# Kernel optimization log

Measured on AMD Instinct MI355X. Metric: run time of the kernel, lower is better.

The kernel has to match this reference:

```python
import jax, jax.numpy as jnp
import numpy as np
import math

HEADS = 2
DH = 64
INNER = HEADS * DH  # 128
TOPK = 128
ALPHA = 10.0
N_FREQ = 8  # feature_dim // (2*input_dim) = 64 // 8
OMEGAS = jnp.logspace(1.0, math.log10(128.0), N_FREQ)           # sigma_q = 128
OMEGAS_L = [jnp.logspace(1.0, math.log10(s), N_FREQ) for s in (128.0, 32.0)]
LAYER_NUM = 2


def calc_gamma(grid, omegas):
    # grid: (Q, 4) -> (Q, 4*2*n_freq)
    arg = jnp.pi * grid[:, :, None] * omegas[None, None, :]      # (Q,4,n)
    g = jnp.concatenate([jnp.sin(arg), jnp.cos(arg)], axis=-1)   # (Q,4,2n)
    return g.reshape(grid.shape[0], -1)


def setup_inputs() -> dict:
    key = jax.random.key(0)
    ks = jax.random.split(key, 20)
    B, Q, L, HD, FD, OD = 2, 4096, 1024, 256, 64, 1

    def w(k, shape, fan_in):
        return jax.random.normal(k, shape, dtype=jnp.float32) * (1.0 / np.sqrt(fan_in))

    inp = {
        'x': jax.random.uniform(ks[0], (B, Q, 4), dtype=jnp.float32),
        'tokens': jax.random.normal(ks[1], (B, L, HD), dtype=jnp.float32),
        'query_W': w(ks[2], (FD, HD), FD),
        'query_b': jnp.zeros((HD,), jnp.float32),
        'q_W': w(ks[3], (HD, INNER), HD),
        'kv_W': w(ks[4], (HD, 2 * INNER), HD),
        'out_W': w(ks[5], (INNER, HD), INNER),
        'out_b': jnp.zeros((HD,), jnp.float32),
        'band_W': w(ks[6], (LAYER_NUM, FD, HD), FD),
        'band_b': jnp.zeros((LAYER_NUM, HD), jnp.float32),
        'mod_W': w(ks[7], (LAYER_NUM, HD, HD), HD),
        'mod_b': jnp.zeros((LAYER_NUM, HD), jnp.float32),
        'hv_W': w(ks[8], (LAYER_NUM - 1, HD, HD), HD),
        'hv_b': jnp.zeros((LAYER_NUM - 1, HD), jnp.float32),
        'outl_W': w(ks[9], (LAYER_NUM, HD, OD), HD),
        'outl_b': jnp.zeros((LAYER_NUM, OD), jnp.float32),
        'gD': 8, 'gH': 8, 'gW': 8, 'gT': 8,
    }
    return inp


def reference(x, tokens, query_W, query_b, q_W, kv_W, out_W, out_b,
              band_W, band_b, mod_W, mod_b, hv_W, hv_b, outl_W, outl_b,
              gD, gH, gW, gT):
    B, Q, _ = x.shape
    L = tokens.shape[1]
    grid = x[0]  # (Q, 4) — torch code uses x[0] for all batches

    # --- patch index + approximate relative distances -> sparse attn indices ---
    z_i = (grid[:, 0] * gD).astype(jnp.int32)
    y_i = (grid[:, 1] * gH).astype(jnp.int32)
    x_i = (grid[:, 2] * gW).astype(jnp.int32)
    t_i = (grid[:, 3] * gT).astype(jnp.int32)
    idx = ((t_i * gD + z_i) * gH + y_i) * gW + x_i               # (Q,)
    N = gD * gH * gW * gT
    t = idx / N                                                  # (Q,) float
    tok_pos = (jnp.arange(L, dtype=jnp.float32) + 0.5) / L       # (L,)
    bias = ALPHA * (t[:, None] - tok_pos[None, :]) ** 2          # (Q, L)
    # top-k SMALLEST distances (identical across batch, compute once)
    _, attn_idx = jax.lax.top_k(-bias, TOPK)                     # (Q, k)

    # --- query features ---
    gamma_q = calc_gamma(grid, OMEGAS)                           # (Q, 64)
    x_q = jax.nn.relu(gamma_q @ query_W + query_b)               # (Q, 256)
    x_q = jnp.broadcast_to(x_q[None], (B, Q, x_q.shape[-1]))

    # --- sparse shared-token cross attention ---
    scale = DH ** -0.5
    q = (x_q @ q_W).reshape(B, Q, HEADS, DH)                     # (B,Q,H,Dh)
    kv = tokens @ kv_W                                           # (B,L,2*inner)
    k_full, v_full = kv[..., :INNER], kv[..., INNER:]            # (B,L,inner)
    k_sp = k_full[:, attn_idx, :].reshape(B, Q, TOPK, HEADS, DH)  # (B,Q,k,H,Dh)
    v_sp = v_full[:, attn_idx, :].reshape(B, Q, TOPK, HEADS, DH)
    sim = jnp.einsum('bqhd,bqkhd->bhqk', q, k_sp) * scale        # (B,H,Q,k)
    attn = jax.nn.softmax(sim, axis=-1)
    o = jnp.einsum('bhqk,bqkhd->bqhd', attn, v_sp).reshape(B, Q, INNER)
    modulation = o @ out_W + out_b                               # (B,Q,256)

    # --- per-band modulation ---
    mods = []
    for l in range(LAYER_NUM):
        gamma_l = calc_gamma(grid, OMEGAS_L[l])                  # (Q, 64)
        h_l = jax.nn.relu(gamma_l @ band_W[l] + band_b[l])       # (Q, 256)
        m_l = jax.nn.relu(h_l[None] + modulation @ mod_W[l] + mod_b[l])
        mods.append(m_l)

    h_v = [mods[0]]
    for i in range(LAYER_NUM - 1):
        h_v.append(jax.nn.relu((mods[i + 1] + h_v[i]) @ hv_W[i] + hv_b[i]))

    out = sum(h_v[i] @ outl_W[i] + outl_b[i] for i in range(LAYER_NUM))
    return out  # (B, Q, output_dim)
```

## Files before the change

### kernel.cpp

```cpp
#include <hip/hip_runtime.h>
#include <math.h>

#define BN     2
#define QN     4096
#define LN     1024
#define TOPKN  128
#define PI_F   3.14159265358979323846f

#define K_OM0  0.3642064529893673
#define K_OM1  0.1661644014008115

#define NCMAX  320
#define PFP    328

typedef __attribute__((ext_vector_type(8))) short  s16x8;
typedef __attribute__((ext_vector_type(4))) short  s16x4;
typedef __attribute__((ext_vector_type(4))) float  f32x4;
typedef unsigned short u16;

__device__ __forceinline__ u16 f2bf(float f) {
    unsigned int u = __float_as_uint(f);
    u = (u + 0x7FFFu + ((u >> 16) & 1u)) >> 16;
    return (u16)u;
}

__device__ __forceinline__ size_t wtile(int n, int k, int K) {
    return (size_t)((n >> 4) * (K >> 5) + (k >> 5)) * 512 + (n & 15) * 32 + (k & 31);
}
__device__ __forceinline__ size_t kidx(int b, int l, int d) {
    return (((size_t)(b * 64 + (l >> 4)) * 16 + (d >> 3)) * 16 + (l & 15)) * 8 + (d & 7);
}
__device__ __forceinline__ size_t vidx(int b, int n, int k) {
    return (((size_t)(b * 8 + (n >> 4)) * 128 + (k >> 3)) * 16 + (n & 15)) * 8 + (k & 7);
}

struct KvS { u16 tok[32 * 264]; u16 stage[256 * 40]; float vtile[128][40]; };
struct QS  { float shx[128]; u16 gam[32 * 72]; u16 xq[32 * 264]; u16 stage[256 * 40]; };
struct TrS { float tile[32][33]; };
struct SoS { int hist[1024]; int cur[1024]; };
union PrepS { KvS kv; QS q; TrS tr; SoS so; };

__global__ __launch_bounds__(1024) void prep_kernel(
    const float* __restrict__ tokens, const float* __restrict__ kv_W,
    const float* __restrict__ x, const float* __restrict__ query_W,
    const float* __restrict__ query_b, const float* __restrict__ q_W,
    const float* __restrict__ outW, const float* __restrict__ bandW,
    const float* __restrict__ modW, const float* __restrict__ hvW,
    const int* __restrict__ gDp, const int* __restrict__ gHp,
    const int* __restrict__ gWp, const int* __restrict__ gTp,
    float* __restrict__ qall, u16* __restrict__ kbf, u16* __restrict__ vtbf,
    u16* __restrict__ outT, u16* __restrict__ bandT,
    u16* __restrict__ modT, u16* __restrict__ hvT,
    int* __restrict__ perm, int* __restrict__ ssort)
{
    __shared__ __align__(16) PrepS sm;
    const int bid = blockIdx.x;
    const int t   = threadIdx.x;
    const int wid = t >> 6, lane = t & 63;
    const int quad = lane >> 4, l16 = lane & 15;

    if (bid < 64) {
        int l0 = bid * 32;
        int b = l0 >> 10, lloc = l0 & 1023;
        #pragma unroll
        for (int i = 0; i < 8; i++) {
            int idx = i * 1024 + t; int row = idx >> 8, col = idx & 255;
            sm.kv.tok[row * 264 + col] = f2bf(tokens[(size_t)(l0 + row) * 256 + col]);
        }
        int m0 = (wid & 1) * 16;
        int c0 = (wid >> 1) * 32;
        f32x4 acc[2];
        acc[0] = (f32x4){0.f, 0.f, 0.f, 0.f};
        acc[1] = (f32x4){0.f, 0.f, 0.f, 0.f};
        for (int kc = 0; kc < 8; kc++) {
            __syncthreads();
            #pragma unroll
            for (int i = 0; i < 8; i++) {
                int idx = i * 1024 + t; int k = idx >> 8, n = idx & 255;
                sm.kv.stage[n * 40 + k] = f2bf(kv_W[(size_t)(kc * 32 + k) * 256 + n]);
            }
            __syncthreads();
            s16x8 a = *(const s16x8*)&sm.kv.tok[(m0 + l16) * 264 + kc * 32 + quad * 8];
            #pragma unroll
            for (int sub = 0; sub < 2; sub++) {
                s16x8 bfr = *(const s16x8*)&sm.kv.stage[(c0 + sub * 16 + l16) * 40 + quad * 8];
                acc[sub] = __builtin_amdgcn_mfma_f32_16x16x32_bf16(a, bfr, acc[sub], 0, 0, 0);
            }
        }
        #pragma unroll
        for (int sub = 0; sub < 2; sub++) {
            int col = c0 + sub * 16 + l16;
            if (col < 128) {
                #pragma unroll
                for (int r = 0; r < 4; r++) {
                    int lg = l0 + m0 + quad * 4 + r;
                    kbf[kidx(lg >> 10, lg & 1023, col)] = f2bf(acc[sub][r]);
                }
            } else {
                #pragma unroll
                for (int r = 0; r < 4; r++)
                    sm.kv.vtile[col - 128][m0 + quad * 4 + r] = acc[sub][r];
            }
        }
        __syncthreads();
        {
            int col = t >> 3, rg = (t & 7) * 4;
            float4 v4 = *(const float4*)&sm.kv.vtile[col][rg];
            s16x4 pk;
            pk[0] = (short)f2bf(v4.x); pk[1] = (short)f2bf(v4.y);
            pk[2] = (short)f2bf(v4.z); pk[3] = (short)f2bf(v4.w);
            *(s16x4*)&vtbf[vidx(b, col, lloc + rg)] = pk;
        }
    } else if (bid < 192) {
        int p0 = (bid - 64) * 32;
        if (t < 128) sm.q.shx[t] = x[p0 * 4 + t];
        __syncthreads();
        #pragma unroll
        for (int j = 0; j < 2; j++) {
            int e = t * 2 + j;
            int g = e >> 6, f = e & 63;
            int c = f >> 4, jj = f & 15, oi = jj & 7;
            float om = (float)(10.0 * exp((double)oi * K_OM0));
            float arg = PI_F * sm.q.shx[g * 4 + c] * om;
            sm.q.gam[g * 72 + f] = f2bf((jj < 8) ? sinf(arg) : cosf(arg));
        }
        int m0 = (wid & 1) * 16;
        {
            int c0 = (wid >> 1) * 32;
            f32x4 acc[2];
            acc[0] = (f32x4){0.f, 0.f, 0.f, 0.f};
            acc[1] = (f32x4){0.f, 0.f, 0.f, 0.f};
            for (int kc = 0; kc < 2; kc++) {
                __syncthreads();
                #pragma unroll
                for (int i = 0; i < 8; i++) {
                    int idx = i * 1024 + t; int k = idx >> 8, n = idx & 255;
                    sm.q.stage[n * 40 + k] = f2bf(query_W[(size_t)(kc * 32 + k) * 256 + n]);
                }
                __syncthreads();
                s16x8 a = *(const s16x8*)&sm.q.gam[(m0 + l16) * 72 + kc * 32 + quad * 8];
                #pragma unroll
                for (int sub = 0; sub < 2; sub++) {
                    s16x8 bfr = *(const s16x8*)&sm.q.stage[(c0 + sub * 16 + l16) * 40 + quad * 8];
                    acc[sub] = __builtin_amdgcn_mfma_f32_16x16x32_bf16(a, bfr, acc[sub], 0, 0, 0);
                }
            }
            #pragma unroll
            for (int sub = 0; sub < 2; sub++) {
                int col = c0 + sub * 16 + l16;
                float bias = query_b[col];
                #pragma unroll
                for (int r = 0; r < 4; r++)
                    sm.q.xq[(m0 + quad * 4 + r) * 264 + col] = f2bf(fmaxf(acc[sub][r] + bias, 0.f));
            }
        }
        {
            int n0q = (wid >> 1) * 16;
            f32x4 acc2 = (f32x4){0.f, 0.f, 0.f, 0.f};
            for (int kc = 0; kc < 8; kc++) {
                __syncthreads();
                #pragma unroll
                for (int i = 0; i < 4; i++) {
                    int idx = i * 1024 + t; int k = idx >> 7, n = idx & 127;
                    sm.q.stage[n * 40 + k] = f2bf(q_W[(size_t)(kc * 32 + k) * 128 + n]);
                }
                __syncthreads();
                s16x8 a = *(const s16x8*)&sm.q.xq[(m0 + l16) * 264 + kc * 32 + quad * 8];
                s16x8 bfr = *(const s16x8*)&sm.q.stage[(n0q + l16) * 40 + quad * 8];
                acc2 = __builtin_amdgcn_mfma_f32_16x16x32_bf16(a, bfr, acc2, 0, 0, 0);
            }
            #pragma unroll
            for (int r = 0; r < 4; r++)
                qall[(size_t)(p0 + m0 + quad * 4 + r) * 128 + n0q + l16] = acc2[r];
        }
    } else if (bid < 448) {
        int bid2 = bid - 192;
        const float* src; u16* dst; int K, N, lt;
        if      (bid2 < 32)  { src = outW;  dst = outT;  K = 128; N = 256; lt = bid2; }
        else if (bid2 < 64)  { src = bandW; dst = bandT; K = 128; N = 256; lt = bid2 - 32; }
        else if (bid2 < 192) { src = modW;  dst = modT;  K = 512; N = 256; lt = bid2 - 64; }
        else                 { src = hvW;   dst = hvT;   K = 256; N = 256; lt = bid2 - 192; }
        int tk = K >> 5;
        int ktile = lt % tk, nt = lt / tk;
        int k0 = ktile * 32, n0 = nt * 32;
        int tx = t & 31, ty = (t >> 5) & 31;
        sm.tr.tile[ty][tx] = src[(size_t)(k0 + ty) * N + n0 + tx];
        __syncthreads();
        dst[wtile(n0 + ty, k0 + tx, K)] = f2bf(sm.tr.tile[tx][ty]);
    } else {
        int gD = gDp[0], gH = gHp[0], gW = gWp[0], gT = gTp[0];
        int Ng = gD * gH * gW * gT;
        sm.so.hist[t] = 0;
        __syncthreads();
        int sarr[4];
        #pragma unroll
        for (int i = 0; i < 4; i++) {
            int q = i * 1024 + t;
            float4 xv = *(const float4*)&x[q * 4];
            int zi = (int)(xv.x * (float)gD);
            int yi = (int)(xv.y * (float)gH);
            int xi = (int)(xv.z * (float)gW);
            int ti = (int)(xv.w * (float)gT);
            int idx = ((ti * gD + zi) * gH + yi) * gW + xi;
            float tt = (float)idx / (float)Ng;
            int s = (int)ceilf(tt * (float)LN - ((float)(TOPKN / 2) + 0.5f));
            s = min(max(s, 0), LN - TOPKN);
            sarr[i] = s;
            atomicAdd(&sm.so.hist[s], 1);
        }
        __syncthreads();
        int cnt = sm.so.hist[t];
        sm.so.cur[t] = cnt;
        __syncthreads();
        for (int off = 1; off < 1024; off <<= 1) {
            int u = (t >= off) ? sm.so.cur[t - off] : 0;
            __syncthreads();
            sm.so.cur[t] += u;
            __syncthreads();
        }
        int excl = sm.so.cur[t] - cnt;
        __syncthreads();
        sm.so.hist[t] = excl;
        __syncthreads();
        #pragma unroll
        for (int i = 0; i < 4; i++) {
            int q = i * 1024 + t;
            int pos = atomicAdd(&sm.so.hist[sarr[i]], 1);
            perm[pos] = q;
            ssort[pos] = sarr[i];
        }
    }
}

__global__ __launch_bounds__(1024, 8) void fused_kernel(
    const float* __restrict__ x,
    const u16* __restrict__ kbf, const u16* __restrict__ vtbf,
    const float* __restrict__ qall,
    const int* __restrict__ perm, const int* __restrict__ ssort,
    const u16* __restrict__ outT, const float* __restrict__ out_b,
    const u16* __restrict__ bandT, const float* __restrict__ band_b,
    const u16* __restrict__ modT, const float* __restrict__ mod_b,
    const u16* __restrict__ hvT, const float* __restrict__ hv_b,
    const float* __restrict__ outl_W, const float* __restrict__ outl_b,
    float* __restrict__ out)
{
    const int bid = blockIdx.x;
    const int b   = bid >> 8;
    const int sp0 = (bid & 255) * 16;
    const int t   = threadIdx.x;
    const int wid = t >> 6, lane = t & 63;
    const int quad = lane >> 4, l16 = lane & 15;

    __shared__ __align__(16) u16 q_bf[16 * 136];
    __shared__ __align__(16) u16 gam_lds[32 * 72];
    __shared__ __align__(16) u16 P_bf[32 * PFP];
    __shared__ __align__(16) unsigned char regionA[PFP * 16 * 4];
    __shared__ __align__(16) u16 o_lds[16 * 136];
    __shared__ float fin[256];
    __shared__ float sh_xc[64];
    __shared__ int sh_pq[16], sh_s[16];

    float* P_f32 = (float*)regionA;
    float* o_part = (float*)regionA;
    u16* modu_lds = (u16*)regionA;
    u16* s01_lds  = (u16*)(regionA + 16 * 264 * 2);

    if (t < 16) { sh_pq[t] = perm[sp0 + t]; sh_s[t] = ssort[sp0 + t]; }
    __syncthreads();

    {
        int m = t >> 6, d = (t & 63) * 2;
        float2 qv = *(const float2*)&qall[(size_t)sh_pq[m] * 128 + d];
        unsigned int pk = (unsigned int)f2bf(qv.x) | ((unsigned int)f2bf(qv.y) << 16);
        *(unsigned int*)&q_bf[m * 136 + d] = pk;
    }
    if (t < 64) sh_xc[t] = x[(size_t)sh_pq[t >> 2] * 4 + (t & 3)];
    __syncthreads();

    #pragma unroll
    for (int j = 0; j < 2; j++) {
        int e = t * 2 + j;
        int l = e >> 10, g = (e >> 6) & 15, f = e & 63;
        int c = f >> 4, jj = f & 15, oi = jj & 7;
        float om = (float)(10.0 * exp((double)oi * (l ? K_OM1 : K_OM0)));
        float arg = PI_F * sh_xc[g * 4 + c] * om;
        gam_lds[(l * 16 + g) * 72 + f] = f2bf((jj < 8) ? sinf(arg) : cosf(arg));
    }

    const int u0    = sh_s[0] & ~15;
    const int ncols = min((sh_s[15] + 128 - u0 + 31) & ~31, NCMAX);
    const int nsub  = ncols >> 4;
    const int nkc   = ncols >> 5;

    #pragma unroll
    for (int h = 0; h < 2; h++) {
        s16x8 aq0 = *(const s16x8*)&q_bf[l16 * 136 + h * 64 + quad * 8];
        s16x8 aq1 = *(const s16x8*)&q_bf[l16 * 136 + h * 64 + 32 + quad * 8];
        for (int sub = wid; sub < nsub; sub += 16) {
            f32x4 acc = (f32x4){0.f, 0.f, 0.f, 0.f};
            int lrow = u0 + sub * 16 + l16;
            s16x8 b0 = *(const s16x8*)&kbf[kidx(b, lrow, h * 64 + quad * 8)];
            s16x8 b1 = *(const s16x8*)&kbf[kidx(b, lrow, h * 64 + 32 + quad * 8)];
            acc = __builtin_amdgcn_mfma_f32_16x16x32_bf16(aq0, b0, acc, 0, 0, 0);
            acc = __builtin_amdgcn_mfma_f32_16x16x32_bf16(aq1, b1, acc, 0, 0, 0);
            #pragma unroll
            for (int r = 0; r < 4; r++)
                P_f32[(quad * 4 + r) * PFP + sub * 16 + l16] = acc[r];
        }
        __syncthreads();
        {
            int g = wid;
            int sg = sh_s[g];
            float vals[5]; int ok[5];
            float mx = -1e30f;
            #pragma unroll
            for (int i = 0; i < 5; i++) {
                int c = lane + 64 * i;
                float v = P_f32[g * PFP + c] * 0.125f;
                int key = u0 + c;
                int o2 = (c < ncols) && (key >= sg) && (key < sg + 128);
                vals[i] = v; ok[i] = o2;
                if (o2) mx = fmaxf(mx, v);
            }
            #pragma unroll
            for (int off = 1; off < 64; off <<= 1) mx = fmaxf(mx, __shfl_xor(mx, off));
            float sum = 0.f, e5[5];
            #pragma unroll
            for (int i = 0; i < 5; i++) {
                float e = ok[i] ? expf(vals[i] - mx) : 0.f;
                e5[i] = e; sum += e;
            }
            #pragma unroll
            for (int off = 1; off < 64; off <<= 1) sum += __shfl_xor(sum, off);
            float inv = 1.f / sum;
            #pragma unroll
            for (int i = 0; i < 5; i++) {
                int c = lane + 64 * i;
                if (c < ncols) P_bf[(h * 16 + g) * PFP + c] = f2bf(e5[i] * inv);
            }
        }
        __syncthreads();
    }

    {
        int n0 = (wid & 7) * 16;
        int hh = n0 >> 6;
        int khalf = wid >> 3;
        int nk2 = (nkc + 1) >> 1;
        int k0 = khalf ? nk2 : 0;
        int k1 = khalf ? nkc : nk2;
        f32x4 acc = (f32x4){0.f, 0.f, 0.f, 0.f};
        for (int kc = k0; kc < k1; kc++) {
            s16x8 a = *(const s16x8*)&P_bf[(hh * 16 + l16) * PFP + kc * 32 + quad * 8];
            int koff = u0 + kc * 32 + quad * 8;
            koff = min(koff, 1016);
            s16x8 bfr = *(const s16x8*)&vtbf[vidx(b, n0 + l16, koff)];
            acc = __builtin_amdgcn_mfma_f32_16x16x32_bf16(a, bfr, acc, 0, 0, 0);
        }
        #pragma unroll
        for (int r = 0; r < 4; r++)
            o_part[(khalf * 16 + quad * 4 + r) * 128 + n0 + l16] = acc[r];
    }
    __syncthreads();

    {
        int m = t >> 6, j2 = (t & 63) * 2;
        float v0 = o_part[m * 128 + j2]     + o_part[(16 + m) * 128 + j2];
        float v1 = o_part[m * 128 + j2 + 1] + o_part[(16 + m) * 128 + j2 + 1];
        unsigned int pk = (unsigned int)f2bf(v0) | ((unsigned int)f2bf(v1) << 16);
        *(unsigned int*)&o_lds[m * 136 + j2] = pk;
    }
    __syncthreads();

    const int n0 = wid * 16;
    float m0f[4];

    {
        f32x4 acc = (f32x4){0.f, 0.f, 0.f, 0.f};
        #pragma unroll
        for (int kc = 0; kc < 4; kc++) {
            s16x8 a = *(const s16x8*)&o_lds[l16 * 136 + kc * 32 + quad * 8];
            s16x8 bfr = *(const s16x8*)&outT[wtile(n0 + l16, kc * 32 + quad * 8, 128)];
            acc = __builtin_amdgcn_mfma_f32_16x16x32_bf16(a, bfr, acc, 0, 0, 0);
        }
        int col = n0 + l16;
        float bias = out_b[col];
        #pragma unroll
        for (int r = 0; r < 4; r++)
            modu_lds[(quad * 4 + r) * 264 + col] = f2bf(acc[r] + bias);
    }
    __syncthreads();

    #pragma unroll
    for (int l = 0; l < 2; l++) {
        f32x4 acc1 = (f32x4){0.f, 0.f, 0.f, 0.f};
        f32x4 acc2 = (f32x4){0.f, 0.f, 0.f, 0.f};
        #pragma unroll
        for (int kc = 0; kc < 2; kc++) {
            s16x8 a = *(const s16x8*)&gam_lds[(l * 16 + l16) * 72 + kc * 32 + quad * 8];
            s16x8 bfr = *(const s16x8*)&bandT[wtile(n0 + l16, l * 64 + kc * 32 + quad * 8, 128)];
            acc1 = __builtin_amdgcn_mfma_f32_16x16x32_bf16(a, bfr, acc1, 0, 0, 0);
        }
        #pragma unroll
        for (int kc = 0; kc < 8; kc++) {
            s16x8 a = *(const s16x8*)&modu_lds[l16 * 264 + kc * 32 + quad * 8];
            s16x8 bfr = *(const s16x8*)&modT[wtile(n0 + l16, l * 256 + kc * 32 + quad * 8, 512)];
            acc2 = __builtin_amdgcn_mfma_f32_16x16x32_bf16(a, bfr, acc2, 0, 0, 0);
        }
        int col = n0 + l16;
        float bb = band_b[l * 256 + col];
        float mb = mod_b[l * 256 + col];
        #pragma unroll
        for (int r = 0; r < 4; r++) {
            float hval = fmaxf(acc1[r] + bb, 0.f);
            float mval = fmaxf(hval + acc2[r] + mb, 0.f);
            if (l == 0) m0f[r] = mval;
            else s01_lds[(quad * 4 + r) * 264 + col] = f2bf(m0f[r] + mval);
        }
    }
    __syncthreads();

    {
        f32x4 acc = (f32x4){0.f, 0.f, 0.f, 0.f};
        #pragma unroll
        for (int kc = 0; kc < 8; kc++) {
            s16x8 a = *(const s16x8*)&s01_lds[l16 * 264 + kc * 32 + quad * 8];
            s16x8 bfr = *(const s16x8*)&hvT[wtile(n0 + l16, kc * 32 + quad * 8, 256)];
            acc = __builtin_amdgcn_mfma_f32_16x16x32_bf16(a, bfr, acc, 0, 0, 0);
        }
        int col = n0 + l16;
        float w0 = outl_W[col], w1 = outl_W[256 + col], hb = hv_b[col];
        #pragma unroll
        for (int r = 0; r < 4; r++) {
            float hvv = fmaxf(acc[r] + hb, 0.f);
            float pv = m0f[r] * w0 + hvv * w1;
            #pragma unroll
            for (int off = 1; off < 16; off <<= 1) pv += __shfl_xor(pv, off);
            if (l16 == 0) fin[wid * 16 + quad * 4 + r] = pv;
        }
    }
    __syncthreads();
    if (t < 16) {
        float s2 = outl_b[0] + outl_b[1];
        #pragma unroll
        for (int w = 0; w < 16; w++) s2 += fin[w * 16 + t];
        out[(size_t)b * QN + sh_pq[t]] = s2;
    }
}

extern "C" void kernel_launch(void* const* d_in, const int* in_sizes, int n_in,
                              void* d_out, int out_size, void* d_ws, size_t ws_size,
                              hipStream_t stream)
{
    const float* x       = (const float*)d_in[0];
    const float* tokens  = (const float*)d_in[1];
    const float* query_W = (const float*)d_in[2];
    const float* query_b = (const float*)d_in[3];
    const float* q_W     = (const float*)d_in[4];
    const float* kv_W    = (const float*)d_in[5];
    const float* out_W   = (const float*)d_in[6];
    const float* out_b   = (const float*)d_in[7];
    const float* band_W  = (const float*)d_in[8];
    const float* band_b  = (const float*)d_in[9];
    const float* mod_W   = (const float*)d_in[10];
    const float* mod_b   = (const float*)d_in[11];
    const float* hv_W    = (const float*)d_in[12];
    const float* hv_b    = (const float*)d_in[13];
    const float* outl_W  = (const float*)d_in[14];
    const float* outl_b  = (const float*)d_in[15];
    const int*   gD      = (const int*)d_in[16];
    const int*   gH      = (const int*)d_in[17];
    const int*   gW      = (const int*)d_in[18];
    const int*   gT      = (const int*)d_in[19];

    float* ws   = (float*)d_ws;
    float* qall = ws;
    u16* wb = (u16*)(ws + 524288);
    u16* kbf   = wb;
    u16* vtbf  = wb + 262144;
    u16* outT  = wb + 524288;
    u16* bandT = wb + 557056;
    u16* modT  = wb + 589824;
    u16* hvT   = wb + 720896;
    int* perm  = (int*)(wb + 786432);
    int* ssort = perm + 4096;
    float* out = (float*)d_out;

    prep_kernel<<<449, 1024, 0, stream>>>(tokens, kv_W, x, query_W, query_b, q_W,
                                          out_W, band_W, mod_W, hv_W,
                                          gD, gH, gW, gT,
                                          qall, kbf, vtbf, outT, bandT, modT, hvT,
                                          perm, ssort);
    fused_kernel<<<512, 1024, 0, stream>>>(x, kbf, vtbf, qall, perm, ssort,
        outT, out_b, bandT, band_b, modT, mod_b, hvT, hv_b,
        outl_W, outl_b, out);
}
```

Measured before the change: 130.0 us.

## Merge per-head score and softmax passes and drop split-K PV reduction

Both heads' QK score tiles are now computed in one loop into a single 32-row fp32 LDS buffer, followed by one softmax pass, which removes two barriers per block. Softmax probabilities are written as bf16 in place over the fp32 scores. The PV matmul drops its split-K across 16 waves: only 8 waves run the full K loop and write bf16 output directly, which removes the partial-sum buffer, the reduction step and one barrier. The trade-off is that half the waves sit idle during PV and each active wave runs a longer serial K loop.

```diff
diff --git a/kernel.cpp b/kernel.cpp
--- a/kernel.cpp
+++ b/kernel.cpp
@@ -253,17 +253,14 @@
 
     __shared__ __align__(16) u16 q_bf[16 * 136];
     __shared__ __align__(16) u16 gam_lds[32 * 72];
-    __shared__ __align__(16) u16 P_bf[32 * PFP];
-    __shared__ __align__(16) unsigned char regionA[PFP * 16 * 4];
+    __shared__ __align__(16) float scores32[32 * PFP];
     __shared__ __align__(16) u16 o_lds[16 * 136];
     __shared__ float fin[256];
     __shared__ float sh_xc[64];
     __shared__ int sh_pq[16], sh_s[16];
 
-    float* P_f32 = (float*)regionA;
-    float* o_part = (float*)regionA;
-    u16* modu_lds = (u16*)regionA;
-    u16* s01_lds  = (u16*)(regionA + 16 * 264 * 2);
+    u16* modu_lds = (u16*)scores32;
+    u16* s01_lds  = ((u16*)scores32) + 16 * 264;
 
     if (t < 16) { sh_pq[t] = perm[sp0 + t]; sh_s[t] = ssort[sp0 + t]; }
     __syncthreads();
@@ -292,31 +289,39 @@
     const int nsub  = ncols >> 4;
     const int nkc   = ncols >> 5;
 
-    #pragma unroll
-    for (int h = 0; h < 2; h++) {
-        s16x8 aq0 = *(const s16x8*)&q_bf[l16 * 136 + h * 64 + quad * 8];
-        s16x8 aq1 = *(const s16x8*)&q_bf[l16 * 136 + h * 64 + 32 + quad * 8];
-        for (int sub = wid; sub < nsub; sub += 16) {
+    {
+        s16x8 aq00 = *(const s16x8*)&q_bf[l16 * 136 + quad * 8];
+        s16x8 aq01 = *(const s16x8*)&q_bf[l16 * 136 + 32 + quad * 8];
+        s16x8 aq10 = *(const s16x8*)&q_bf[l16 * 136 + 64 + quad * 8];
+        s16x8 aq11 = *(const s16x8*)&q_bf[l16 * 136 + 96 + quad * 8];
+        for (int j = wid; j < 2 * nsub; j += 16) {
+            int h = (j >= nsub) ? 1 : 0;
+            int sub = j - h * nsub;
+            int lrow = u0 + sub * 16 + l16;
             f32x4 acc = (f32x4){0.f, 0.f, 0.f, 0.f};
-            int lrow = u0 + sub * 16 + l16;
             s16x8 b0 = *(const s16x8*)&kbf[kidx(b, lrow, h * 64 + quad * 8)];
             s16x8 b1 = *(const s16x8*)&kbf[kidx(b, lrow, h * 64 + 32 + quad * 8)];
-            acc = __builtin_amdgcn_mfma_f32_16x16x32_bf16(aq0, b0, acc, 0, 0, 0);
-            acc = __builtin_amdgcn_mfma_f32_16x16x32_bf16(aq1, b1, acc, 0, 0, 0);
+            acc = __builtin_amdgcn_mfma_f32_16x16x32_bf16(h ? aq10 : aq00, b0, acc, 0, 0, 0);
+            acc = __builtin_amdgcn_mfma_f32_16x16x32_bf16(h ? aq11 : aq01, b1, acc, 0, 0, 0);
             #pragma unroll
             for (int r = 0; r < 4; r++)
-                P_f32[(quad * 4 + r) * PFP + sub * 16 + l16] = acc[r];
-        }
-        __syncthreads();
-        {
-            int g = wid;
-            int sg = sh_s[g];
+                scores32[(h * 16 + quad * 4 + r) * PFP + sub * 16 + l16] = acc[r];
+        }
+    }
+    __syncthreads();
+
+    {
+        int g = wid;
+        int sg = sh_s[g];
+        #pragma unroll
+        for (int rr = 0; rr < 2; rr++) {
+            int row = g + rr * 16;
             float vals[5]; int ok[5];
             float mx = -1e30f;
             #pragma unroll
             for (int i = 0; i < 5; i++) {
                 int c = lane + 64 * i;
-                float v = P_f32[g * PFP + c] * 0.125f;
+                float v = scores32[row * PFP + c] * 0.125f;
                 int key = u0 + c;
                 int o2 = (c < ncols) && (key >= sg) && (key < sg + 128);
                 vals[i] = v; ok[i] = o2;
@@ -333,25 +338,23 @@
             #pragma unroll
             for (int off = 1; off < 64; off <<= 1) sum += __shfl_xor(sum, off);
             float inv = 1.f / sum;
+            u16* prow = (u16*)&scores32[row * PFP];
             #pragma unroll
             for (int i = 0; i < 5; i++) {
                 int c = lane + 64 * i;
-                if (c < ncols) P_bf[(h * 16 + g) * PFP + c] = f2bf(e5[i] * inv);
-            }
-        }
-        __syncthreads();
-    }
-
-    {
-        int n0 = (wid & 7) * 16;
+                if (c < ncols) prow[c] = f2bf(e5[i] * inv);
+            }
+        }
+    }
+    __syncthreads();
+
+    if (wid < 8) {
+        int n0 = wid * 16;
         int hh = n0 >> 6;
-        int khalf = wid >> 3;
-        int nk2 = (nkc + 1) >> 1;
-        int k0 = khalf ? nk2 : 0;
-        int k1 = khalf ? nkc : nk2;
+        const u16* prow = (const u16*)&scores32[(hh * 16 + l16) * PFP];
         f32x4 acc = (f32x4){0.f, 0.f, 0.f, 0.f};
-        for (int kc = k0; kc < k1; kc++) {
-            s16x8 a = *(const s16x8*)&P_bf[(hh * 16 + l16) * PFP + kc * 32 + quad * 8];
+        for (int kc = 0; kc < nkc; kc++) {
+            s16x8 a = *(const s16x8*)&prow[kc * 32 + quad * 8];
             int koff = u0 + kc * 32 + quad * 8;
             koff = min(koff, 1016);
             s16x8 bfr = *(const s16x8*)&vtbf[vidx(b, n0 + l16, koff)];
@@ -359,16 +362,7 @@
         }
         #pragma unroll
         for (int r = 0; r < 4; r++)
-            o_part[(khalf * 16 + quad * 4 + r) * 128 + n0 + l16] = acc[r];
-    }
-    __syncthreads();
-
-    {
-        int m = t >> 6, j2 = (t & 63) * 2;
-        float v0 = o_part[m * 128 + j2]     + o_part[(16 + m) * 128 + j2];
-        float v1 = o_part[m * 128 + j2 + 1] + o_part[(16 + m) * 128 + j2 + 1];
-        unsigned int pk = (unsigned int)f2bf(v0) | ((unsigned int)f2bf(v1) << 16);
-        *(unsigned int*)&o_lds[m * 136 + j2] = pk;
+            o_lds[(quad * 4 + r) * 136 + n0 + l16] = f2bf(acc[r]);
     }
     __syncthreads();
 
```

Measured after the change: 128.1 us. No clear change (-1.5%).
